# Kernel tuning notes

Hardware: AMD Instinct MI355X
Metric: run time of the kernel (lower is better)

Reference implementation:

```python
import jax, jax.numpy as jnp
import numpy as np

N = 50000        # n_nodes
E = 800000       # edges per graph (avg degree 16)
D_IN = 256       # n_input
D1, D2, D3 = 128, 64, 20   # gae_n_enc_1/2/3
K = 10           # n_clusters
V = 1.0          # student-t dof


def gnn_layer(x, W, src, dst, w):
    # support = x @ W ; out = spmm(adj, support) ; leaky_relu(0.2)
    support = x @ W                          # [N, out]
    msg = w[:, None] * support[src]          # [E, out] gather
    out = jax.ops.segment_sum(msg, dst, num_segments=N)  # scatter-add
    return jax.nn.leaky_relu(out, negative_slope=0.2)


def setup_inputs() -> dict:
    key = jax.random.key(0)
    ks = jax.random.split(key, 32)
    d = {}
    d['topology_feature'] = jax.random.normal(ks[0], (N, D_IN), jnp.float32)
    d['geo_feature'] = jax.random.normal(ks[1], (N, D_IN), jnp.float32)
    d['text_feature'] = jax.random.normal(ks[2], (N, D_IN), jnp.float32)
    for i, name in enumerate(['topo', 'geo', 'text']):
        d[name + '_src'] = jax.random.randint(ks[3 + 3 * i], (E,), 0, N, jnp.int32)
        d[name + '_dst'] = jax.random.randint(ks[4 + 3 * i], (E,), 0, N, jnp.int32)
        d[name + '_w'] = jax.random.uniform(ks[5 + 3 * i], (E,), jnp.float32)
    # learned parameters (xavier-ish scale)
    def xavier(k, fan_in, fan_out):
        s = jnp.sqrt(6.0 / (fan_in + fan_out)).astype(jnp.float32)
        return jax.random.uniform(k, (fan_in, fan_out), jnp.float32, -s, s)
    dims = [(D_IN, D1), (D1, D2), (D2, D3)]
    kk = 12
    for br in ['topo', 'geo', 'text']:
        for li, (fi, fo) in enumerate(dims, start=1):
            d[f'W_{br}{li}'] = xavier(ks[kk], fi, fo)
            kk += 1
    d['cluster_layer'] = xavier(ks[kk], K, D3)
    return d


def reference(topology_feature, geo_feature, text_feature,
              topo_src, topo_dst, topo_w,
              geo_src, geo_dst, geo_w,
              text_src, text_dst, text_w,
              W_topo1, W_topo2, W_topo3,
              W_geo1, W_geo2, W_geo3,
              W_text1, W_text2, W_text3,
              cluster_layer):
    z1 = (gnn_layer(topology_feature, W_topo1, topo_src, topo_dst, topo_w)
          + gnn_layer(geo_feature, W_geo1, geo_src, geo_dst, geo_w)
          + gnn_layer(text_feature, W_text1, text_src, text_dst, text_w)) / 3.0
    z2 = (gnn_layer(z1, W_topo2, topo_src, topo_dst, topo_w)
          + gnn_layer(z1, W_geo2, geo_src, geo_dst, geo_w)
          + gnn_layer(z1, W_text2, text_src, text_dst, text_w)) / 3.0
    z = (gnn_layer(z2, W_topo3, topo_src, topo_dst, topo_w)
         + gnn_layer(z2, W_geo3, geo_src, geo_dst, geo_w)
         + gnn_layer(z2, W_text3, text_src, text_dst, text_w)) / 3.0
    # Student-t soft assignment
    dist = jnp.sum((z[:, None, :] - cluster_layer[None, :, :]) ** 2, axis=2)  # [N,K]
    q = 1.0 / (1.0 + dist / V)
    q = q ** ((V + 1.0) / 2.0)
    q = q / jnp.sum(q, axis=1, keepdims=True)
    return (z, q)
```

## Files before the change

### kernel.cpp

```cpp
#include <hip/hip_runtime.h>

#define D_IN 256

typedef __bf16 bf16x8 __attribute__((ext_vector_type(8)));
typedef float f32x4 __attribute__((ext_vector_type(4)));

static __device__ __forceinline__ ushort f2b(float f) {
    uint u = __float_as_uint(f);
    u += 0x7FFF + ((u >> 16) & 1);
    return (ushort)(u >> 16);
}
static __device__ __forceinline__ float b2f(ushort h) {
    return __uint_as_float(((uint)h) << 16);
}
static __device__ __forceinline__ float lrelu(float v) {
    return (v >= 0.f) ? v : 0.2f * v;
}

__global__ void hist3_kernel(const int* __restrict__ d0, const int* __restrict__ d1,
                             const int* __restrict__ d2, int* __restrict__ hist,
                             int E, int N) {
    int g = blockIdx.y;
    const int* d = (g == 0) ? d0 : (g == 1) ? d1 : d2;
    int i = blockIdx.x * blockDim.x + threadIdx.x;
    if (i < E) atomicAdd(&hist[g * N + d[i]], 1);
}

__global__ __launch_bounds__(1024) void scan3_kernel(int* __restrict__ hist,
                                                     int* __restrict__ row_ptr,
                                                     int N) {
    int g = blockIdx.x;
    int* h = hist + g * N;
    int* rp = row_ptr + g * (N + 1);
    __shared__ int partial[1024];
    int tid = threadIdx.x;
    int chunk = (N + 1023) >> 10;
    int beg = tid * chunk;
    int end = min(beg + chunk, N);
    int s = 0;
    for (int i = beg; i < end; ++i) s += h[i];
    partial[tid] = s;
    __syncthreads();
    for (int off = 1; off < 1024; off <<= 1) {
        int v = (tid >= off) ? partial[tid - off] : 0;
        __syncthreads();
        partial[tid] += v;
        __syncthreads();
    }
    int run = (tid == 0) ? 0 : partial[tid - 1];
    for (int i = beg; i < end; ++i) {
        int hv = h[i];
        rp[i] = run;
        h[i] = run;
        run += hv;
    }
    if (tid == 1023) rp[N] = partial[1023];
}

__global__ void scatter3_kernel(const int* __restrict__ s0, const int* __restrict__ s1,
                                const int* __restrict__ s2, const int* __restrict__ d0,
                                const int* __restrict__ d1, const int* __restrict__ d2,
                                const float* __restrict__ w0, const float* __restrict__ w1,
                                const float* __restrict__ w2, int* __restrict__ cursor,
                                int* __restrict__ csr_src, float* __restrict__ csr_w,
                                int E, int N) {
    int g = blockIdx.y;
    const int* src = (g == 0) ? s0 : (g == 1) ? s1 : s2;
    const int* dst = (g == 0) ? d0 : (g == 1) ? d1 : d2;
    const float* w = (g == 0) ? w0 : (g == 1) ? w1 : w2;
    int i = blockIdx.x * blockDim.x + threadIdx.x;
    if (i < E) {
        int d = dst[i];
        int pos = atomicAdd(&cursor[g * N + d], 1);
        csr_src[(size_t)g * E + pos] = src[i];
        csr_w[(size_t)g * E + pos] = w[i];
    }
}

template <int K, int NC, int NCP>
__global__ void prep_kernel(const float* __restrict__ W0, const float* __restrict__ W1,
                            const float* __restrict__ W2, ushort* __restrict__ Wt) {
    int g = blockIdx.y;
    const float* W = (g == 0) ? W0 : (g == 1) ? W1 : W2;
    ushort* o = Wt + (size_t)g * NCP * K;
    for (int idx = blockIdx.x * 256 + threadIdx.x; idx < NCP * K; idx += gridDim.x * 256) {
        int c = idx / K, k = idx - c * K;
        float v = (c < NC) ? W[(size_t)k * NC + c] : 0.f;
        o[idx] = f2b(v);
    }
}

template <int K, int NCP>
__global__ __launch_bounds__(256) void gemm_kernel(const float* __restrict__ A,
                                                   const ushort* __restrict__ Wt,
                                                   ushort* __restrict__ C, int M) {
    constexpr int WAVES_N = (NCP >= 128) ? 2 : 1;
    constexpr int WAVES_M = 4 / WAVES_N;
    constexpr int WM = 128 / WAVES_M;
    constexpr int WN = NCP / WAVES_N;
    constexpr int FM = WM / 16;
    constexpr int FN = WN / 16;

    __shared__ ushort As[128 * 40];
    __shared__ ushort Bs[NCP * 40];

    int tid = threadIdx.x;
    int lane = tid & 63;
    int wave = tid >> 6;
    int lo = lane & 15, hi = lane >> 4;
    int wm0, wn0;
    if (WAVES_N == 2) { wm0 = (wave >> 1) * WM; wn0 = (wave & 1) * WN; }
    else              { wm0 = wave * WM;        wn0 = 0; }
    int row0 = blockIdx.x * 128;

    f32x4 acc[FM][FN];
#pragma unroll
    for (int i = 0; i < FM; ++i)
#pragma unroll
        for (int j = 0; j < FN; ++j) acc[i][j] = (f32x4){0.f, 0.f, 0.f, 0.f};

    for (int k0 = 0; k0 < K; k0 += 32) {
        __syncthreads();
#pragma unroll
        for (int i = 0; i < 4; ++i) {
            int f = tid + 256 * i;
            int r = f >> 3, kc = f & 7;
            float4 v = make_float4(0.f, 0.f, 0.f, 0.f);
            if (row0 + r < M)
                v = *(const float4*)&A[(size_t)(row0 + r) * K + k0 + kc * 4];
            ushort4 u;
            u.x = f2b(v.x); u.y = f2b(v.y); u.z = f2b(v.z); u.w = f2b(v.w);
            *(ushort4*)&As[r * 40 + kc * 4] = u;
        }
        for (int idx = tid; idx < NCP * 4; idx += 256) {
            int c = idx >> 2, q = idx & 3;
            *(uint4*)&Bs[c * 40 + q * 8] = *(const uint4*)&Wt[(size_t)c * K + k0 + q * 8];
        }
        __syncthreads();

        bf16x8 afr[FM], bfr[FN];
#pragma unroll
        for (int fm = 0; fm < FM; ++fm)
            afr[fm] = *(const bf16x8*)&As[(wm0 + fm * 16 + lo) * 40 + 8 * hi];
#pragma unroll
        for (int fn = 0; fn < FN; ++fn)
            bfr[fn] = *(const bf16x8*)&Bs[(wn0 + fn * 16 + lo) * 40 + 8 * hi];
#pragma unroll
        for (int fm = 0; fm < FM; ++fm)
#pragma unroll
            for (int fn = 0; fn < FN; ++fn)
                acc[fm][fn] = __builtin_amdgcn_mfma_f32_16x16x32_bf16(
                    afr[fm], bfr[fn], acc[fm][fn], 0, 0, 0);
    }

#pragma unroll
    for (int fm = 0; fm < FM; ++fm)
#pragma unroll
        for (int fn = 0; fn < FN; ++fn)
#pragma unroll
            for (int r = 0; r < 4; ++r) {
                int row = row0 + wm0 + fm * 16 + hi * 4 + r;
                if (row < M)
                    C[(size_t)row * NCP + wn0 + fn * 16 + lo] = f2b(acc[fm][fn][r]);
            }
}

template <int DS, int LPN, bool OUT20>
__global__ __launch_bounds__(256) void agg3_kernel(const ushort* __restrict__ sup,
                                                   const int* __restrict__ rowptr,
                                                   const int* __restrict__ csrsrc,
                                                   const float* __restrict__ csrw,
                                                   float* __restrict__ z, int N, int E) {
    int t = blockIdx.x * 256 + threadIdx.x;
    int n = t / LPN;
    int sub = t - n * LPN;
    if (n >= N) return;
    float t0 = 0.f, t1 = 0.f, t2 = 0.f, t3 = 0.f;
#pragma unroll
    for (int g = 0; g < 3; ++g) {
        const int* rp = rowptr + g * (N + 1);
        const int* cs = csrsrc + (size_t)g * E;
        const float* cw = csrw + (size_t)g * E;
        const ushort* sg = sup + (size_t)g * N * DS;
        int beg = rp[n], end = rp[n + 1];
        float a0 = 0.f, a1 = 0.f, a2 = 0.f, a3 = 0.f;
        for (int e = beg; e < end; ++e) {
            int s = cs[e];
            float w = cw[e];
            ushort4 v = *(const ushort4*)&sg[(size_t)s * DS + sub * 4];
            a0 += w * b2f(v.x);
            a1 += w * b2f(v.y);
            a2 += w * b2f(v.z);
            a3 += w * b2f(v.w);
        }
        t0 += lrelu(a0); t1 += lrelu(a1); t2 += lrelu(a2); t3 += lrelu(a3);
    }
    const float s3 = 1.f / 3.f;
    if (OUT20) {
        if (sub < 5) {
            float4 o = make_float4(t0 * s3, t1 * s3, t2 * s3, t3 * s3);
            *(float4*)&z[(size_t)n * 20 + sub * 4] = o;
        }
    } else {
        float4 o = make_float4(t0 * s3, t1 * s3, t2 * s3, t3 * s3);
        *(float4*)&z[(size_t)n * DS + sub * 4] = o;
    }
}

__global__ void q_kernel(const float* __restrict__ z, const float* __restrict__ cl,
                         float* __restrict__ qout, int N) {
    __shared__ float c[200];
    if (threadIdx.x < 200) c[threadIdx.x] = cl[threadIdx.x];
    __syncthreads();
    int n = blockIdx.x * blockDim.x + threadIdx.x;
    if (n >= N) return;
    float zr[20];
#pragma unroll
    for (int d = 0; d < 20; ++d) zr[d] = z[(size_t)n * 20 + d];
    float qs[10];
    float sum = 0.f;
#pragma unroll
    for (int k = 0; k < 10; ++k) {
        float dist = 0.f;
#pragma unroll
        for (int d = 0; d < 20; ++d) {
            float t = zr[d] - c[k * 20 + d];
            dist += t * t;
        }
        float qk = 1.0f / (1.0f + dist);
        qs[k] = qk;
        sum += qk;
    }
    float inv = 1.0f / sum;
#pragma unroll
    for (int k = 0; k < 10; ++k) qout[(size_t)n * 10 + k] = qs[k] * inv;
}

extern "C" void kernel_launch(void* const* d_in, const int* in_sizes, int n_in,
                              void* d_out, int out_size, void* d_ws, size_t ws_size,
                              hipStream_t stream) {
    const float* feat[3] = {(const float*)d_in[0], (const float*)d_in[1], (const float*)d_in[2]};
    const int*   srcs[3] = {(const int*)d_in[3], (const int*)d_in[6], (const int*)d_in[9]};
    const int*   dsts[3] = {(const int*)d_in[4], (const int*)d_in[7], (const int*)d_in[10]};
    const float* ews[3]  = {(const float*)d_in[5], (const float*)d_in[8], (const float*)d_in[11]};
    const float* Wp[3][3];
    for (int b = 0; b < 3; ++b)
        for (int l = 0; l < 3; ++l)
            Wp[b][l] = (const float*)d_in[12 + 3 * b + l];
    const float* cluster = (const float*)d_in[21];

    const int N = in_sizes[0] / D_IN;
    const int E = in_sizes[3];

    size_t off = 0;
    auto take = [&](size_t bytes) -> void* {
        void* p = (char*)d_ws + off;
        off += (bytes + 255) & ~(size_t)255;
        return p;
    };
    int*    cursor = (int*)take((size_t)3 * N * 4);
    int*    rowptr = (int*)take((size_t)3 * (N + 1) * 4);
    int*    csrsrc = (int*)take((size_t)3 * E * 4);
    float*  csrw   = (float*)take((size_t)3 * E * 4);
    ushort* wt1    = (ushort*)take((size_t)3 * 128 * 256 * 2);
    ushort* wt2    = (ushort*)take((size_t)3 * 64 * 128 * 2);
    ushort* wt3    = (ushort*)take((size_t)3 * 32 * 64 * 2);
    ushort* sup    = (ushort*)take((size_t)3 * N * 128 * 2);
    float*  z1     = (float*)take((size_t)N * 128 * 4);
    float*  z2     = (float*)take((size_t)N * 64 * 4);
    (void)ws_size;

    float* zout = (float*)d_out;
    float* qout = zout + (size_t)N * 20;

    hipMemsetAsync(cursor, 0, (size_t)3 * N * 4, stream);
    int gE = (E + 255) / 256;
    hist3_kernel<<<dim3(gE, 3), 256, 0, stream>>>(dsts[0], dsts[1], dsts[2], cursor, E, N);
    scan3_kernel<<<3, 1024, 0, stream>>>(cursor, rowptr, N);
    scatter3_kernel<<<dim3(gE, 3), 256, 0, stream>>>(srcs[0], srcs[1], srcs[2],
                                                     dsts[0], dsts[1], dsts[2],
                                                     ews[0], ews[1], ews[2],
                                                     cursor, csrsrc, csrw, E, N);

    prep_kernel<256, 128, 128><<<dim3(32, 3), 256, 0, stream>>>(Wp[0][0], Wp[1][0], Wp[2][0], wt1);
    prep_kernel<128, 64, 64><<<dim3(16, 3), 256, 0, stream>>>(Wp[0][1], Wp[1][1], Wp[2][1], wt2);
    prep_kernel<64, 20, 32><<<dim3(8, 3), 256, 0, stream>>>(Wp[0][2], Wp[1][2], Wp[2][2], wt3);

    int gM = (N + 127) / 128;

    for (int b = 0; b < 3; ++b)
        gemm_kernel<256, 128><<<gM, 256, 0, stream>>>(feat[b], wt1 + (size_t)b * 128 * 256,
                                                      sup + (size_t)b * N * 128, N);
    agg3_kernel<128, 32, false><<<(N * 32 + 255) / 256, 256, 0, stream>>>(
        sup, rowptr, csrsrc, csrw, z1, N, E);

    for (int b = 0; b < 3; ++b)
        gemm_kernel<128, 64><<<gM, 256, 0, stream>>>(z1, wt2 + (size_t)b * 64 * 128,
                                                     sup + (size_t)b * N * 64, N);
    agg3_kernel<64, 16, false><<<(N * 16 + 255) / 256, 256, 0, stream>>>(
        sup, rowptr, csrsrc, csrw, z2, N, E);

    for (int b = 0; b < 3; ++b)
        gemm_kernel<64, 32><<<gM, 256, 0, stream>>>(z2, wt3 + (size_t)b * 32 * 64,
                                                    sup + (size_t)b * N * 32, N);
    agg3_kernel<32, 8, true><<<(N * 8 + 255) / 256, 256, 0, stream>>>(
        sup, rowptr, csrsrc, csrw, zout, N, E);

    q_kernel<<<(N + 255) / 256, 256, 0, stream>>>(zout, cluster, qout, N);
}
```

Measured before the change: 957.7 us.

## Pack CSR edges, batch branch GEMMs, widen aggregation to 8 features per lane

Source index and weight are packed into one int2 record per edge, so aggregation does a single 8-byte load per edge instead of two separate array reads. Layer 1 runs its three branch GEMMs in one launch via a grid y-dimension. Layers 2 and 3 concatenate the three branch weights into a single wider GEMM (192 and 96 output columns), so the shared input is read once. The aggregation kernel now has each lane handle 8 bf16 features with 16-byte gathers and processes two edges per iteration. Fewer lanes per node mean more serial work per thread and possibly lower occupancy.

```diff
diff --git a/kernel.cpp b/kernel.cpp
--- a/kernel.cpp
+++ b/kernel.cpp
@@ -10,8 +10,11 @@
     u += 0x7FFF + ((u >> 16) & 1);
     return (ushort)(u >> 16);
 }
-static __device__ __forceinline__ float b2f(ushort h) {
-    return __uint_as_float(((uint)h) << 16);
+static __device__ __forceinline__ float blo(uint u) {
+    return __uint_as_float(u << 16);
+}
+static __device__ __forceinline__ float bhi(uint u) {
+    return __uint_as_float(u & 0xffff0000u);
 }
 static __device__ __forceinline__ float lrelu(float v) {
     return (v >= 0.f) ? v : 0.2f * v;
@@ -62,8 +65,7 @@
                                 const int* __restrict__ d1, const int* __restrict__ d2,
                                 const float* __restrict__ w0, const float* __restrict__ w1,
                                 const float* __restrict__ w2, int* __restrict__ cursor,
-                                int* __restrict__ csr_src, float* __restrict__ csr_w,
-                                int E, int N) {
+                                int2* __restrict__ csre, int E, int N) {
     int g = blockIdx.y;
     const int* src = (g == 0) ? s0 : (g == 1) ? s1 : s2;
     const int* dst = (g == 0) ? d0 : (g == 1) ? d1 : d2;
@@ -72,34 +74,40 @@
     if (i < E) {
         int d = dst[i];
         int pos = atomicAdd(&cursor[g * N + d], 1);
-        csr_src[(size_t)g * E + pos] = src[i];
-        csr_w[(size_t)g * E + pos] = w[i];
-    }
-}
-
-template <int K, int NC, int NCP>
+        unsigned long long rec = ((unsigned long long)(uint)__float_as_int(w[i]) << 32)
+                               | (uint)src[i];
+        __builtin_nontemporal_store(rec, (unsigned long long*)&csre[(size_t)g * E + pos]);
+    }
+}
+
+template <int K, int NC, int NCP_PER>
 __global__ void prep_kernel(const float* __restrict__ W0, const float* __restrict__ W1,
                             const float* __restrict__ W2, ushort* __restrict__ Wt) {
-    int g = blockIdx.y;
+    int idx = blockIdx.x * 256 + threadIdx.x;
+    if (idx >= 3 * NCP_PER * K) return;
+    int row = idx / K, k = idx - row * K;
+    int g = row / NCP_PER, cc = row - g * NCP_PER;
     const float* W = (g == 0) ? W0 : (g == 1) ? W1 : W2;
-    ushort* o = Wt + (size_t)g * NCP * K;
-    for (int idx = blockIdx.x * 256 + threadIdx.x; idx < NCP * K; idx += gridDim.x * 256) {
-        int c = idx / K, k = idx - c * K;
-        float v = (c < NC) ? W[(size_t)k * NC + c] : 0.f;
-        o[idx] = f2b(v);
-    }
-}
-
-template <int K, int NCP>
-__global__ __launch_bounds__(256) void gemm_kernel(const float* __restrict__ A,
+    Wt[idx] = f2b(cc < NC ? W[(size_t)k * NC + cc] : 0.f);
+}
+
+template <int K, int NCP, bool B3>
+__global__ __launch_bounds__(256) void gemm_kernel(const float* __restrict__ A0,
+                                                   const float* __restrict__ A1,
+                                                   const float* __restrict__ A2,
                                                    const ushort* __restrict__ Wt,
                                                    ushort* __restrict__ C, int M) {
-    constexpr int WAVES_N = (NCP >= 128) ? 2 : 1;
-    constexpr int WAVES_M = 4 / WAVES_N;
-    constexpr int WM = 128 / WAVES_M;
-    constexpr int WN = NCP / WAVES_N;
-    constexpr int FM = WM / 16;
-    constexpr int FN = WN / 16;
+    constexpr int FM = 4;
+    constexpr int FN = NCP / 32;
+    const float* A = A0;
+    const ushort* Wtg = Wt;
+    ushort* Cg = C;
+    if (B3) {
+        int g = blockIdx.y;
+        A = (g == 0) ? A0 : (g == 1) ? A1 : A2;
+        Wtg = Wt + (size_t)g * NCP * K;
+        Cg = C + (size_t)g * (size_t)M * NCP;
+    }
 
     __shared__ ushort As[128 * 40];
     __shared__ ushort Bs[NCP * 40];
@@ -108,9 +116,8 @@
     int lane = tid & 63;
     int wave = tid >> 6;
     int lo = lane & 15, hi = lane >> 4;
-    int wm0, wn0;
-    if (WAVES_N == 2) { wm0 = (wave >> 1) * WM; wn0 = (wave & 1) * WN; }
-    else              { wm0 = wave * WM;        wn0 = 0; }
+    int wm0 = (wave >> 1) * 64;
+    int wn0 = (wave & 1) * (NCP / 2);
     int row0 = blockIdx.x * 128;
 
     f32x4 acc[FM][FN];
@@ -134,7 +141,7 @@
         }
         for (int idx = tid; idx < NCP * 4; idx += 256) {
             int c = idx >> 2, q = idx & 3;
-            *(uint4*)&Bs[c * 40 + q * 8] = *(const uint4*)&Wt[(size_t)c * K + k0 + q * 8];
+            *(uint4*)&Bs[c * 40 + q * 8] = *(const uint4*)&Wtg[(size_t)c * K + k0 + q * 8];
         }
         __syncthreads();
 
@@ -161,49 +168,81 @@
             for (int r = 0; r < 4; ++r) {
                 int row = row0 + wm0 + fm * 16 + hi * 4 + r;
                 if (row < M)
-                    C[(size_t)row * NCP + wn0 + fn * 16 + lo] = f2b(acc[fm][fn][r]);
+                    Cg[(size_t)row * NCP + wn0 + fn * 16 + lo] = f2b(acc[fm][fn][r]);
             }
 }
 
-template <int DS, int LPN, bool OUT20>
+template <int LPN, bool OUT20>
 __global__ __launch_bounds__(256) void agg3_kernel(const ushort* __restrict__ sup,
                                                    const int* __restrict__ rowptr,
-                                                   const int* __restrict__ csrsrc,
-                                                   const float* __restrict__ csrw,
-                                                   float* __restrict__ z, int N, int E) {
+                                                   const int2* __restrict__ csre,
+                                                   float* __restrict__ z, int N, int E,
+                                                   int gstride, int rowstride) {
     int t = blockIdx.x * 256 + threadIdx.x;
     int n = t / LPN;
     int sub = t - n * LPN;
     if (n >= N) return;
-    float t0 = 0.f, t1 = 0.f, t2 = 0.f, t3 = 0.f;
+
+    float tot[8];
+#pragma unroll
+    for (int j = 0; j < 8; ++j) tot[j] = 0.f;
+
 #pragma unroll
     for (int g = 0; g < 3; ++g) {
-        const int* rp = rowptr + g * (N + 1);
-        const int* cs = csrsrc + (size_t)g * E;
-        const float* cw = csrw + (size_t)g * E;
-        const ushort* sg = sup + (size_t)g * N * DS;
-        int beg = rp[n], end = rp[n + 1];
-        float a0 = 0.f, a1 = 0.f, a2 = 0.f, a3 = 0.f;
-        for (int e = beg; e < end; ++e) {
-            int s = cs[e];
-            float w = cw[e];
-            ushort4 v = *(const ushort4*)&sg[(size_t)s * DS + sub * 4];
-            a0 += w * b2f(v.x);
-            a1 += w * b2f(v.y);
-            a2 += w * b2f(v.z);
-            a3 += w * b2f(v.w);
-        }
-        t0 += lrelu(a0); t1 += lrelu(a1); t2 += lrelu(a2); t3 += lrelu(a3);
-    }
+        const int2* ce = csre + (size_t)g * E;
+        int beg = rowptr[g * (N + 1) + n];
+        int end = rowptr[g * (N + 1) + n + 1];
+        const ushort* sg = sup + (size_t)g * gstride + (size_t)sub * 8;
+        float a[8];
+#pragma unroll
+        for (int j = 0; j < 8; ++j) a[j] = 0.f;
+        int e = beg;
+        for (; e + 1 < end; e += 2) {
+            int2 e0 = ce[e];
+            int2 e1 = ce[e + 1];
+            uint4 v0 = *(const uint4*)&sg[(size_t)e0.x * rowstride];
+            uint4 v1 = *(const uint4*)&sg[(size_t)e1.x * rowstride];
+            float w0 = __int_as_float(e0.y);
+            float w1 = __int_as_float(e1.y);
+            a[0] += w0 * blo(v0.x); a[1] += w0 * bhi(v0.x);
+            a[2] += w0 * blo(v0.y); a[3] += w0 * bhi(v0.y);
+            a[4] += w0 * blo(v0.z); a[5] += w0 * bhi(v0.z);
+            a[6] += w0 * blo(v0.w); a[7] += w0 * bhi(v0.w);
+            a[0] += w1 * blo(v1.x); a[1] += w1 * bhi(v1.x);
+            a[2] += w1 * blo(v1.y); a[3] += w1 * bhi(v1.y);
+            a[4] += w1 * blo(v1.z); a[5] += w1 * bhi(v1.z);
+            a[6] += w1 * blo(v1.w); a[7] += w1 * bhi(v1.w);
+        }
+        if (e < end) {
+            int2 e0 = ce[e];
+            uint4 v0 = *(const uint4*)&sg[(size_t)e0.x * rowstride];
+            float w0 = __int_as_float(e0.y);
+            a[0] += w0 * blo(v0.x); a[1] += w0 * bhi(v0.x);
+            a[2] += w0 * blo(v0.y); a[3] += w0 * bhi(v0.y);
+            a[4] += w0 * blo(v0.z); a[5] += w0 * bhi(v0.z);
+            a[6] += w0 * blo(v0.w); a[7] += w0 * bhi(v0.w);
+        }
+#pragma unroll
+        for (int j = 0; j < 8; ++j) tot[j] += lrelu(a[j]);
+    }
+
     const float s3 = 1.f / 3.f;
+#pragma unroll
+    for (int j = 0; j < 8; ++j) tot[j] *= s3;
+
     if (OUT20) {
-        if (sub < 5) {
-            float4 o = make_float4(t0 * s3, t1 * s3, t2 * s3, t3 * s3);
-            *(float4*)&z[(size_t)n * 20 + sub * 4] = o;
+        int f0 = sub * 8;
+        if (f0 < 20) {
+            *(float4*)&z[(size_t)n * 20 + f0] =
+                make_float4(tot[0], tot[1], tot[2], tot[3]);
+            if (f0 + 4 < 20)
+                *(float4*)&z[(size_t)n * 20 + f0 + 4] =
+                    make_float4(tot[4], tot[5], tot[6], tot[7]);
         }
     } else {
-        float4 o = make_float4(t0 * s3, t1 * s3, t2 * s3, t3 * s3);
-        *(float4*)&z[(size_t)n * DS + sub * 4] = o;
+        float* zr = &z[(size_t)n * (8 * LPN) + sub * 8];
+        *(float4*)&zr[0] = make_float4(tot[0], tot[1], tot[2], tot[3]);
+        *(float4*)&zr[4] = make_float4(tot[4], tot[5], tot[6], tot[7]);
     }
 }
 
@@ -260,8 +299,7 @@
     };
     int*    cursor = (int*)take((size_t)3 * N * 4);
     int*    rowptr = (int*)take((size_t)3 * (N + 1) * 4);
-    int*    csrsrc = (int*)take((size_t)3 * E * 4);
-    float*  csrw   = (float*)take((size_t)3 * E * 4);
+    int2*   csre   = (int2*)take((size_t)3 * E * 8);
     ushort* wt1    = (ushort*)take((size_t)3 * 128 * 256 * 2);
     ushort* wt2    = (ushort*)take((size_t)3 * 64 * 128 * 2);
     ushort* wt3    = (ushort*)take((size_t)3 * 32 * 64 * 2);
@@ -280,31 +318,29 @@
     scatter3_kernel<<<dim3(gE, 3), 256, 0, stream>>>(srcs[0], srcs[1], srcs[2],
                                                      dsts[0], dsts[1], dsts[2],
                                                      ews[0], ews[1], ews[2],
-                                                     cursor, csrsrc, csrw, E, N);
-
-    prep_kernel<256, 128, 128><<<dim3(32, 3), 256, 0, stream>>>(Wp[0][0], Wp[1][0], Wp[2][0], wt1);
-    prep_kernel<128, 64, 64><<<dim3(16, 3), 256, 0, stream>>>(Wp[0][1], Wp[1][1], Wp[2][1], wt2);
-    prep_kernel<64, 20, 32><<<dim3(8, 3), 256, 0, stream>>>(Wp[0][2], Wp[1][2], Wp[2][2], wt3);
+                                                     cursor, csre, E, N);
+
+    prep_kernel<256, 128, 128><<<(3 * 128 * 256 + 255) / 256, 256, 0, stream>>>(
+        Wp[0][0], Wp[1][0], Wp[2][0], wt1);
+    prep_kernel<128, 64, 64><<<(3 * 64 * 128 + 255) / 256, 256, 0, stream>>>(
+        Wp[0][1], Wp[1][1], Wp[2][1], wt2);
+    prep_kernel<64, 20, 32><<<(3 * 32 * 64 + 255) / 256, 256, 0, stream>>>(
+        Wp[0][2], Wp[1][2], Wp[2][2], wt3);
 
     int gM = (N + 127) / 128;
 
-    for (int b = 0; b < 3; ++b)
-        gemm_kernel<256, 128><<<gM, 256, 0, stream>>>(feat[b], wt1 + (size_t)b * 128 * 256,
-                                                      sup + (size_t)b * N * 128, N);
-    agg3_kernel<128, 32, false><<<(N * 32 + 255) / 256, 256, 0, stream>>>(
-        sup, rowptr, csrsrc, csrw, z1, N, E);
-
-    for (int b = 0; b < 3; ++b)
-        gemm_kernel<128, 64><<<gM, 256, 0, stream>>>(z1, wt2 + (size_t)b * 64 * 128,
-                                                     sup + (size_t)b * N * 64, N);
-    agg3_kernel<64, 16, false><<<(N * 16 + 255) / 256, 256, 0, stream>>>(
-        sup, rowptr, csrsrc, csrw, z2, N, E);
-
-    for (int b = 0; b < 3; ++b)
-        gemm_kernel<64, 32><<<gM, 256, 0, stream>>>(z2, wt3 + (size_t)b * 32 * 64,
-                                                    sup + (size_t)b * N * 32, N);
-    agg3_kernel<32, 8, true><<<(N * 8 + 255) / 256, 256, 0, stream>>>(
-        sup, rowptr, csrsrc, csrw, zout, N, E);
+    gemm_kernel<256, 128, true><<<dim3(gM, 3), 256, 0, stream>>>(
+        feat[0], feat[1], feat[2], wt1, sup, N);
+    agg3_kernel<16, false><<<(N * 16 + 255) / 256, 256, 0, stream>>>(
+        sup, rowptr, csre, z1, N, E, N * 128, 128);
+
+    gemm_kernel<128, 192, false><<<gM, 256, 0, stream>>>(z1, z1, z1, wt2, sup, N);
+    agg3_kernel<8, false><<<(N * 8 + 255) / 256, 256, 0, stream>>>(
+        sup, rowptr, csre, z2, N, E, 64, 192);
+
+    gemm_kernel<64, 96, false><<<gM, 256, 0, stream>>>(z2, z2, z2, wt3, sup, N);
+    agg3_kernel<4, true><<<(N * 4 + 255) / 256, 256, 0, stream>>>(
+        sup, rowptr, csre, zout, N, E, 32, 96);
 
     q_kernel<<<(N + 255) / 256, 256, 0, stream>>>(zout, cluster, qout, N);
 }
```

Result: faster. 841.0 us (-12.2%).
